# Kernel tuning notes

Hardware: AMD Instinct MI355X
Metric: run time of the kernel (lower is better)

## Reference

```python
import jax, jax.numpy as jnp
import numpy as np
from jax import lax

T_MAX, BATCH, CLASSES, L_MAX = 512, 32, 1296, 64
NINF = -jnp.inf


def _align_one(logsm, label, C, R):
    """Monotonic max-probability forced alignment for one sample.
    logsm: [T, V] log-probs, label: [L] int, C=x_len (valid frames), R=label_len.
    Returns per-frame pseudo target [T] (0-padded past C)."""
    T, V = logsm.shape
    L = label.shape[0]
    rows = jnp.arange(L)
    cols = jnp.arange(T)
    # pb[i, j] = logsm[j, label[i]], restricted to the monotonic band i <= j <= C-R+i
    pb = logsm[:, label].T  # [L, T]
    band = (cols[None, :] >= rows[:, None]) & (cols[None, :] <= C - R + rows[:, None]) & (rows[:, None] < R)
    pb = jnp.where(band, pb, NINF)

    # Forward DP over time columns: dp[i,j] = max(dp[i-1,j-1], dp[i,j-1]) + pb[i,j]
    # (strict > for the diagonal move, exactly as the original numpy code).
    dp0 = jnp.where(rows == 0, pb[:, 0], NINF)

    def step(dp, pb_col):
        shifted = jnp.concatenate([jnp.full((1,), NINF, dp.dtype), dp[:-1]])
        choice = shifted > dp  # True -> came from (i-1, j-1)
        dp_new = jnp.where(choice, shifted, dp) + pb_col
        return dp_new, choice

    _, choices = lax.scan(step, dp0, pb.T[1:])  # [T-1, L] bool
    choices = jnp.concatenate([jnp.zeros((1, L), bool), choices], axis=0)  # [T, L]

    # Backtrack from (R-1, C-1); columns j >= C emit padding 0.
    def bstep(row, jc):
        j, ch = jc
        active = j < C
        tgt = jnp.where(active, label[row], 0)
        row_new = jnp.where(active, row - ch[row].astype(row.dtype), row)
        return row_new, tgt

    row0 = (R - 1).astype(jnp.int32)
    _, targets = lax.scan(bstep, row0, (jnp.arange(T), choices), reverse=True)
    return targets  # [T]


def _make_targets(logsm, label, x_len, label_len):
    # logsm: [T, B, V] -> targets [T, B]
    return jax.vmap(_align_one, in_axes=(1, 0, 0, 0))(logsm, label, x_len, label_len).T


def setup_inputs() -> dict:
    key = jax.random.key(0)
    k0, k1, k2, k3, k4 = jax.random.split(key, 5)
    pred = jax.random.normal(k0, (T_MAX, BATCH, CLASSES), jnp.float32)
    seq_pred = jax.random.normal(k1, (T_MAX, BATCH, CLASSES), jnp.float32)
    label = jax.random.randint(k2, (BATCH, L_MAX), 0, CLASSES)
    x_len = jax.random.randint(k3, (BATCH,), T_MAX // 2, T_MAX + 1)  # >= L_MAX so band is valid
    label_len = jax.random.randint(k4, (BATCH,), 8, L_MAX + 1)
    return {"pred": pred, "seq_pred": seq_pred, "label": label, "x_len": x_len, "label_len": label_len}


def reference(pred, seq_pred, label, x_len, label_len):
    T, B, V = pred.shape
    logsm_seq = jax.nn.log_softmax(seq_pred, axis=-1)
    target = _make_targets(logsm_seq, label, x_len, label_len)  # [T, B] int
    probs = jnp.exp(logsm_seq)  # softmax(seq_pred)
    conf = jnp.take_along_axis(probs, target[..., None], axis=2)[..., 0]  # [T, B]
    smooth = (1.0 - conf) / (V - 1)
    onehot = jax.nn.one_hot(target, V, dtype=pred.dtype)  # [T, B, V]
    true_dist = jnp.where(onehot > 0, conf[..., None], smooth[..., None])
    mask = (jnp.arange(T)[:, None] < x_len[None, :]).astype(pred.dtype)  # [T, B]
    ce = jnp.sum(-true_dist * jax.nn.log_softmax(pred, axis=-1), axis=-1) * mask
    return jnp.mean(ce)
```

## Files before the change

kernel.cpp:

```cpp
#include <hip/hip_runtime.h>

#define T_MAX 512
#define BATCH 32
#define CLASSES 1296
#define L_MAX 64
#define NROWS (T_MAX * BATCH)
#define NV4 (CLASSES / 4)
#define NINF (-INFINITY)

__device__ __forceinline__ float wave_sum64(float v) {
    v += __int_as_float(__builtin_amdgcn_update_dpp(0, __float_as_int(v), 0x111, 0xF, 0xF, true));
    v += __int_as_float(__builtin_amdgcn_update_dpp(0, __float_as_int(v), 0x112, 0xF, 0xF, true));
    v += __int_as_float(__builtin_amdgcn_update_dpp(0, __float_as_int(v), 0x114, 0xF, 0xF, true));
    v += __int_as_float(__builtin_amdgcn_update_dpp(0, __float_as_int(v), 0x118, 0xF, 0xF, true));
    v += __int_as_float(__builtin_amdgcn_update_dpp(0, __float_as_int(v), 0x142, 0xF, 0xF, true));
    v += __int_as_float(__builtin_amdgcn_update_dpp(0, __float_as_int(v), 0x143, 0xF, 0xF, true));
    return v;
}

__global__ __launch_bounds__(256) void rowstats_kernel(
    const float* __restrict__ pred, const float* __restrict__ seqp,
    const int* __restrict__ label,
    float* __restrict__ lse_pred, float* __restrict__ sum_pred,
    float* __restrict__ lse_seq, float* __restrict__ pb, int* __restrict__ counter)
{
    int r = blockIdx.x * 4 + (threadIdx.x >> 6);
    int lane = threadIdx.x & 63;
    if (r == 0 && lane == 0) *counter = 0;
    const float* xp = pred + (size_t)r * CLASSES;
    const float* xs = seqp + (size_t)r * CLASSES;
    const float4* p4 = (const float4*)xp;
    const float4* s4 = (const float4*)xs;

    float4 a0 = p4[lane],       a1 = p4[lane + 64],  a2 = p4[lane + 128];
    float4 a3 = p4[lane + 192], a4 = p4[lane + 256];
    float4 b0 = s4[lane],       b1 = s4[lane + 64],  b2 = s4[lane + 128];
    float4 b3 = s4[lane + 192], b4 = s4[lane + 256];
    float4 at = make_float4(0.f, 0.f, 0.f, 0.f);
    float4 bt = make_float4(0.f, 0.f, 0.f, 0.f);
    if (lane < 4) { at = p4[320 + lane]; bt = s4[320 + lane]; }
    int lab = label[((r & 31) << 6) + lane];

    float sp = __expf(a0.x) + __expf(a0.y) + __expf(a0.z) + __expf(a0.w)
             + __expf(a1.x) + __expf(a1.y) + __expf(a1.z) + __expf(a1.w)
             + __expf(a2.x) + __expf(a2.y) + __expf(a2.z) + __expf(a2.w)
             + __expf(a3.x) + __expf(a3.y) + __expf(a3.z) + __expf(a3.w)
             + __expf(a4.x) + __expf(a4.y) + __expf(a4.z) + __expf(a4.w);
    float sx = (a0.x + a0.y + a0.z + a0.w) + (a1.x + a1.y + a1.z + a1.w)
             + (a2.x + a2.y + a2.z + a2.w) + (a3.x + a3.y + a3.z + a3.w)
             + (a4.x + a4.y + a4.z + a4.w);
    float ss = __expf(b0.x) + __expf(b0.y) + __expf(b0.z) + __expf(b0.w)
             + __expf(b1.x) + __expf(b1.y) + __expf(b1.z) + __expf(b1.w)
             + __expf(b2.x) + __expf(b2.y) + __expf(b2.z) + __expf(b2.w)
             + __expf(b3.x) + __expf(b3.y) + __expf(b3.z) + __expf(b3.w)
             + __expf(b4.x) + __expf(b4.y) + __expf(b4.z) + __expf(b4.w);
    if (lane < 4) {
        sp += __expf(at.x) + __expf(at.y) + __expf(at.z) + __expf(at.w);
        sx += at.x + at.y + at.z + at.w;
        ss += __expf(bt.x) + __expf(bt.y) + __expf(bt.z) + __expf(bt.w);
    }
    sp = wave_sum64(sp);
    sx = wave_sum64(sx);
    ss = wave_sum64(ss);

    int b = r & 31, t = r >> 5;
    pb[(((size_t)(b << 9) + t) << 6) + lane] = xs[lab];
    if (lane == 63) {
        lse_pred[r] = __logf(sp);
        sum_pred[r] = sx;
        lse_seq[r]  = __logf(ss);
    }
}

__global__ __launch_bounds__(128) void align_kernel(
    const float* __restrict__ pb, const int* __restrict__ x_len,
    const int* __restrict__ label_len, int* __restrict__ tg)
{
    int b = blockIdx.x;
    int tid = threadIdx.x, w = tid >> 6, lane = tid & 63;
    int C = x_len[b], R = label_len[b];
    int limit = C - R;
    __shared__ float buf[2][4096];
    __shared__ uint2 chw[8 * 64];
    __shared__ int a_s[64];
    __shared__ int rows_s[T_MAX];
    const float* pbb = pb + ((size_t)b << 15);
    int P = (C + 63) >> 6;

    int l0 = (lane & 15) << 2;
    bool mk0 = (l0 + 0) < R, mk1 = (l0 + 1) < R, mk2 = (l0 + 2) < R, mk3 = (l0 + 3) < R;
    bool isb0 = (lane & 15) == 0;
    const int ninf_i = 0xFF800000;

    if (w == 1) {
        const float4* s4 = (const float4*)pbb;
        float4* d4 = (float4*)buf[0];
        #pragma unroll
        for (int k = 0; k < 16; ++k) {
            float4 q = s4[(k << 6) + lane];
            q.x = mk0 ? q.x : NINF;  q.y = mk1 ? q.y : NINF;
            q.z = mk2 ? q.z : NINF;  q.w = mk3 ? q.w : NINF;
            d4[(k << 6) + lane] = q;
        }
    }
    __syncthreads();

    float dp = NINF;
    for (int p = 0; p < P; ++p) {
        if (w == 1) {
            int ldp = p + 1; if (ldp > 7) ldp = 7;
            const float4* s4 = (const float4*)(pbb + (ldp << 12));
            float4* d4 = (float4*)buf[(p + 1) & 1];
            #pragma unroll
            for (int k = 0; k < 16; ++k) {
                float4 q = s4[(k << 6) + lane];
                q.x = mk0 ? q.x : NINF;  q.y = mk1 ? q.y : NINF;
                q.z = mk2 ? q.z : NINF;  q.w = mk3 ? q.w : NINF;
                d4[(k << 6) + lane] = q;
            }
        } else {
            const float* bc = buf[p & 1];
            int base = p << 6;
            unsigned w0 = 0, w1 = 0;
            #pragma unroll
            for (int g = 0; g < 4; ++g) {
                float v[16];
                #pragma unroll
                for (int u = 0; u < 16; ++u) v[u] = bc[((g << 4) + u) * 64 + lane];
                bool general = (p == 0) || (base + (g << 4) + 15 > limit);
                #pragma unroll
                for (int u = 0; u < 16; ++u) {
                    int kk = (g << 4) + u;
                    int j = base + kk;
                    float val;
                    if (general) {
                        if (p == 0 && kk == 0) {
                            dp = (lane == 0) ? v[0] : NINF;
                            continue;
                        }
                        bool ib = (lane <= j) && (lane >= j - limit);
                        val = ib ? v[u] : NINF;
                    } else {
                        val = v[u];
                    }
                    int dpb = __float_as_int(dp);
                    int t1 = __builtin_amdgcn_update_dpp(ninf_i, dpb, 0x111, 0xF, 0xF, false);
                    int t2 = __builtin_amdgcn_update_dpp(ninf_i, dpb, 0x142, 0xF, 0xF, false);
                    float shifted = __int_as_float(isb0 ? t2 : t1);
                    bool c = shifted > dp;
                    unsigned bit01 = c ? 1u : 0u;
                    if (kk < 32) w0 |= bit01 << kk; else w1 |= bit01 << (kk - 32);
                    dp = fmaxf(shifted, dp) + val;
                }
            }
            chw[(p << 6) + lane] = make_uint2(w0, w1);
        }
        __syncthreads();
    }

    if (tid == 0) {
        const unsigned* ch32 = (const unsigned*)chw;
        int row = R - 1, j = C - 1;
        while (row > 0 && j >= 0) {
            unsigned word = ch32[((j >> 6) << 7) + (row << 1) + ((j >> 5) & 1)];
            unsigned mb = (2u << (j & 31)) - 1;
            unsigned m = word & mb;
            if (m) {
                int hb = 31 - __clz(m);
                int aj = (j & ~31) | hb;
                a_s[row] = aj;
                row--; j = aj - 1;
            } else {
                j = (j & ~31) - 1;
            }
        }
        for (int i = row; i >= 0; --i) a_s[i] = 0;
    }
    __syncthreads();
    if (tid < R) {
        int a = a_s[tid];
        int bi = (tid == R - 1) ? (C - 1) : (a_s[tid + 1] - 1);
        for (int j = a; j <= bi; ++j) rows_s[j] = tid;
    }
    __syncthreads();
    for (int j = tid; j < T_MAX; j += 128)
        tg[(b << 9) + j] = (j < C) ? rows_s[j] : -1;
}

__global__ __launch_bounds__(256) void ce_kernel(
    const float* __restrict__ pred, const int* __restrict__ label,
    const int* __restrict__ x_len,
    const float* __restrict__ lse_pred, const float* __restrict__ sum_pred,
    const float* __restrict__ lse_seq, const float* __restrict__ pb,
    const int* __restrict__ tg, float* __restrict__ partials,
    int* __restrict__ counter, float* __restrict__ out)
{
    int e = blockIdx.x * 256 + threadIdx.x;
    int t = e >> 5, b = e & 31;
    float ce = 0.f;
    if (t < x_len[b]) {
        int row = tg[(b << 9) + t];
        int tgt = label[(b << 6) + row];
        float lp = lse_pred[e];
        float S = sum_pred[e] - (float)CLASSES * lp;
        float lsp_t = pred[(size_t)e * CLASSES + tgt] - lp;
        float conf = __expf(pb[(((size_t)(b << 9) + t) << 6) + row] - lse_seq[e]);
        float smooth = (1.f - conf) * (1.f / (float)(CLASSES - 1));
        ce = -((conf - smooth) * lsp_t + smooth * S);
    }
    ce = wave_sum64(ce);
    __shared__ float sm[4];
    __shared__ int amLast;
    if ((threadIdx.x & 63) == 63) sm[threadIdx.x >> 6] = ce;
    __syncthreads();
    if (threadIdx.x == 0) {
        float p = sm[0] + sm[1] + sm[2] + sm[3];
        __hip_atomic_store(&partials[blockIdx.x], p, __ATOMIC_RELEASE, __HIP_MEMORY_SCOPE_AGENT);
        amLast = (__hip_atomic_fetch_add(counter, 1, __ATOMIC_ACQ_REL, __HIP_MEMORY_SCOPE_AGENT) == 63);
    }
    __syncthreads();
    if (amLast && threadIdx.x < 64) {
        float v = __hip_atomic_load(&partials[threadIdx.x], __ATOMIC_ACQUIRE, __HIP_MEMORY_SCOPE_AGENT);
        for (int o = 32; o; o >>= 1) v += __shfl_down(v, o, 64);
        if (threadIdx.x == 0) out[0] = v * (1.0f / (float)NROWS);
    }
}

extern "C" void kernel_launch(void* const* d_in, const int* in_sizes, int n_in,
                              void* d_out, int out_size, void* d_ws, size_t ws_size,
                              hipStream_t stream) {
    const float* pred      = (const float*)d_in[0];
    const float* seq_pred  = (const float*)d_in[1];
    const int*   label     = (const int*)d_in[2];
    const int*   x_len     = (const int*)d_in[3];
    const int*   label_len = (const int*)d_in[4];
    float* out = (float*)d_out;

    float* w = (float*)d_ws;
    float* lse_pred = w;
    float* sum_pred = w + NROWS;
    float* lse_seq  = w + 2 * NROWS;
    float* pb       = w + 3 * NROWS;
    int*   tg       = (int*)(w + 3 * NROWS + (size_t)BATCH * T_MAX * 64);
    float* partials = (float*)(tg + NROWS);
    int*   counter  = (int*)(partials + 64);

    rowstats_kernel<<<NROWS / 4, 256, 0, stream>>>(pred, seq_pred, label,
                                                   lse_pred, sum_pred, lse_seq, pb, counter);
    align_kernel<<<BATCH, 128, 0, stream>>>(pb, x_len, label_len, tg);
    ce_kernel<<<64, 256, 0, stream>>>(pred, label, x_len,
                                      lse_pred, sum_pred, lse_seq, pb, tg,
                                      partials, counter, out);
}
```

Baseline: 222.5 us.

## Fuse alignment and CE into one single-wave kernel with async LDS loads

Merges the alignment DP kernel and the cross-entropy kernel into one per-sample kernel, which drops a launch and the target round trip through global memory. The block shrinks to a single wave that prefetches the next tile straight into LDS with global_load_lds, synchronised by s_waitcnt instead of __syncthreads, and it no longer loads tiles past the valid length. Label-length masking moves from the copy into the DP itself as an additive bias. The final reduction becomes one float atomic per sample. This leaves only 32 single-wave blocks doing the CE gather, so little parallelism is available there, and the float atomic adds make the summation order nondeterministic.

Result: slower. 230.2 us (+3.5%).

```diff
diff --git a/kernel.cpp b/kernel.cpp
--- a/kernel.cpp
+++ b/kernel.cpp
@@ -18,15 +18,21 @@
     return v;
 }
 
+__device__ __forceinline__ void glds16(const float* g, float* l) {
+    __builtin_amdgcn_global_load_lds((const __attribute__((address_space(1))) void*)g,
+                                     (__attribute__((address_space(3))) void*)l, 16, 0, 0);
+}
+
 __global__ __launch_bounds__(256) void rowstats_kernel(
     const float* __restrict__ pred, const float* __restrict__ seqp,
     const int* __restrict__ label,
     float* __restrict__ lse_pred, float* __restrict__ sum_pred,
-    float* __restrict__ lse_seq, float* __restrict__ pb, int* __restrict__ counter)
+    float* __restrict__ lse_seq, float* __restrict__ pb,
+    int* __restrict__ counter, float* __restrict__ acc)
 {
     int r = blockIdx.x * 4 + (threadIdx.x >> 6);
     int lane = threadIdx.x & 63;
-    if (r == 0 && lane == 0) *counter = 0;
+    if (r == 0 && lane == 0) { *counter = 0; *acc = 0.f; }
     const float* xp = pred + (size_t)r * CLASSES;
     const float* xs = seqp + (size_t)r * CLASSES;
     const float4* p4 = (const float4*)xp;
@@ -72,93 +78,81 @@
     }
 }
 
-__global__ __launch_bounds__(128) void align_kernel(
-    const float* __restrict__ pb, const int* __restrict__ x_len,
-    const int* __restrict__ label_len, int* __restrict__ tg)
+__global__ __launch_bounds__(64) void align_ce_kernel(
+    const float* __restrict__ pb, const float* __restrict__ pred,
+    const int* __restrict__ label, const int* __restrict__ x_len,
+    const int* __restrict__ label_len,
+    const float* __restrict__ lse_pred, const float* __restrict__ sum_pred,
+    const float* __restrict__ lse_seq,
+    float* __restrict__ acc, int* __restrict__ counter, float* __restrict__ out)
 {
-    int b = blockIdx.x;
-    int tid = threadIdx.x, w = tid >> 6, lane = tid & 63;
+    int b = blockIdx.x, lane = threadIdx.x;
     int C = x_len[b], R = label_len[b];
     int limit = C - R;
     __shared__ float buf[2][4096];
-    __shared__ uint2 chw[8 * 64];
+    __shared__ uint2 chw[512];
+    __shared__ int labs[64];
     __shared__ int a_s[64];
     __shared__ int rows_s[T_MAX];
     const float* pbb = pb + ((size_t)b << 15);
     int P = (C + 63) >> 6;
 
-    int l0 = (lane & 15) << 2;
-    bool mk0 = (l0 + 0) < R, mk1 = (l0 + 1) < R, mk2 = (l0 + 2) < R, mk3 = (l0 + 3) < R;
+    labs[lane] = label[(b << 6) + lane];
+    float biasR = (lane < R) ? 0.f : NINF;
     bool isb0 = (lane & 15) == 0;
     const int ninf_i = 0xFF800000;
 
-    if (w == 1) {
-        const float4* s4 = (const float4*)pbb;
-        float4* d4 = (float4*)buf[0];
-        #pragma unroll
-        for (int k = 0; k < 16; ++k) {
-            float4 q = s4[(k << 6) + lane];
-            q.x = mk0 ? q.x : NINF;  q.y = mk1 ? q.y : NINF;
-            q.z = mk2 ? q.z : NINF;  q.w = mk3 ? q.w : NINF;
-            d4[(k << 6) + lane] = q;
-        }
-    }
-    __syncthreads();
+    #pragma unroll
+    for (int k = 0; k < 16; ++k) glds16(pbb + (k << 8) + lane * 4, &buf[0][k << 8]);
 
     float dp = NINF;
     for (int p = 0; p < P; ++p) {
-        if (w == 1) {
-            int ldp = p + 1; if (ldp > 7) ldp = 7;
-            const float4* s4 = (const float4*)(pbb + (ldp << 12));
-            float4* d4 = (float4*)buf[(p + 1) & 1];
+        int ldp = p + 1; if (ldp >= P) ldp = P - 1;
+        const float* src = pbb + ((size_t)ldp << 12);
+        float* dst = buf[(p + 1) & 1];
+        #pragma unroll
+        for (int k = 0; k < 16; ++k) glds16(src + (k << 8) + lane * 4, &dst[k << 8]);
+        __asm__ __volatile__("s_waitcnt vmcnt(16)" ::: "memory");
+
+        const float* bc = buf[p & 1];
+        int base = p << 6;
+        unsigned w0 = 0, w1 = 0;
+        #pragma unroll
+        for (int g = 0; g < 4; ++g) {
+            float v[16];
             #pragma unroll
-            for (int k = 0; k < 16; ++k) {
-                float4 q = s4[(k << 6) + lane];
-                q.x = mk0 ? q.x : NINF;  q.y = mk1 ? q.y : NINF;
-                q.z = mk2 ? q.z : NINF;  q.w = mk3 ? q.w : NINF;
-                d4[(k << 6) + lane] = q;
+            for (int u = 0; u < 16; ++u) v[u] = bc[((g << 4) + u) * 64 + lane];
+            bool general = (p == 0) || (base + (g << 4) + 15 > limit);
+            #pragma unroll
+            for (int u = 0; u < 16; ++u) {
+                int kk = (g << 4) + u;
+                int j = base + kk;
+                float val;
+                if (general) {
+                    if (p == 0 && kk == 0) {
+                        dp = (lane == 0) ? v[0] : NINF;
+                        continue;
+                    }
+                    bool ib = (lane <= j) && (lane >= j - limit) && (lane < R);
+                    val = ib ? v[u] : NINF;
+                } else {
+                    val = v[u] + biasR;
+                }
+                int dpb = __float_as_int(dp);
+                int t1 = __builtin_amdgcn_update_dpp(ninf_i, dpb, 0x111, 0xF, 0xF, false);
+                int t2 = __builtin_amdgcn_update_dpp(ninf_i, dpb, 0x142, 0xF, 0xF, false);
+                float shifted = __int_as_float(isb0 ? t2 : t1);
+                bool c = shifted > dp;
+                unsigned bit01 = c ? 1u : 0u;
+                if (kk < 32) w0 |= bit01 << kk; else w1 |= bit01 << (kk - 32);
+                dp = fmaxf(shifted, dp) + val;
             }
-        } else {
-            const float* bc = buf[p & 1];
-            int base = p << 6;
-            unsigned w0 = 0, w1 = 0;
-            #pragma unroll
-            for (int g = 0; g < 4; ++g) {
-                float v[16];
-                #pragma unroll
-                for (int u = 0; u < 16; ++u) v[u] = bc[((g << 4) + u) * 64 + lane];
-                bool general = (p == 0) || (base + (g << 4) + 15 > limit);
-                #pragma unroll
-                for (int u = 0; u < 16; ++u) {
-                    int kk = (g << 4) + u;
-                    int j = base + kk;
-                    float val;
-                    if (general) {
-                        if (p == 0 && kk == 0) {
-                            dp = (lane == 0) ? v[0] : NINF;
-                            continue;
-                        }
-                        bool ib = (lane <= j) && (lane >= j - limit);
-                        val = ib ? v[u] : NINF;
-                    } else {
-                        val = v[u];
-                    }
-                    int dpb = __float_as_int(dp);
-                    int t1 = __builtin_amdgcn_update_dpp(ninf_i, dpb, 0x111, 0xF, 0xF, false);
-                    int t2 = __builtin_amdgcn_update_dpp(ninf_i, dpb, 0x142, 0xF, 0xF, false);
-                    float shifted = __int_as_float(isb0 ? t2 : t1);
-                    bool c = shifted > dp;
-                    unsigned bit01 = c ? 1u : 0u;
-                    if (kk < 32) w0 |= bit01 << kk; else w1 |= bit01 << (kk - 32);
-                    dp = fmaxf(shifted, dp) + val;
-                }
-            }
-            chw[(p << 6) + lane] = make_uint2(w0, w1);
-        }
-        __syncthreads();
-    }
-
-    if (tid == 0) {
+        }
+        chw[(p << 6) + lane] = make_uint2(w0, w1);
+    }
+    __asm__ __volatile__("s_waitcnt vmcnt(0)" ::: "memory");
+
+    if (lane == 0) {
         const unsigned* ch32 = (const unsigned*)chw;
         int row = R - 1, j = C - 1;
         while (row > 0 && j >= 0) {
@@ -176,53 +170,52 @@
         }
         for (int i = row; i >= 0; --i) a_s[i] = 0;
     }
-    __syncthreads();
-    if (tid < R) {
-        int a = a_s[tid];
-        int bi = (tid == R - 1) ? (C - 1) : (a_s[tid + 1] - 1);
-        for (int j = a; j <= bi; ++j) rows_s[j] = tid;
-    }
-    __syncthreads();
-    for (int j = tid; j < T_MAX; j += 128)
-        tg[(b << 9) + j] = (j < C) ? rows_s[j] : -1;
-}
-
-__global__ __launch_bounds__(256) void ce_kernel(
-    const float* __restrict__ pred, const int* __restrict__ label,
-    const int* __restrict__ x_len,
-    const float* __restrict__ lse_pred, const float* __restrict__ sum_pred,
-    const float* __restrict__ lse_seq, const float* __restrict__ pb,
-    const int* __restrict__ tg, float* __restrict__ partials,
-    int* __restrict__ counter, float* __restrict__ out)
-{
-    int e = blockIdx.x * 256 + threadIdx.x;
-    int t = e >> 5, b = e & 31;
-    float ce = 0.f;
-    if (t < x_len[b]) {
-        int row = tg[(b << 9) + t];
-        int tgt = label[(b << 6) + row];
-        float lp = lse_pred[e];
-        float S = sum_pred[e] - (float)CLASSES * lp;
-        float lsp_t = pred[(size_t)e * CLASSES + tgt] - lp;
-        float conf = __expf(pb[(((size_t)(b << 9) + t) << 6) + row] - lse_seq[e]);
-        float smooth = (1.f - conf) * (1.f / (float)(CLASSES - 1));
-        ce = -((conf - smooth) * lsp_t + smooth * S);
-    }
-    ce = wave_sum64(ce);
-    __shared__ float sm[4];
-    __shared__ int amLast;
-    if ((threadIdx.x & 63) == 63) sm[threadIdx.x >> 6] = ce;
-    __syncthreads();
-    if (threadIdx.x == 0) {
-        float p = sm[0] + sm[1] + sm[2] + sm[3];
-        __hip_atomic_store(&partials[blockIdx.x], p, __ATOMIC_RELEASE, __HIP_MEMORY_SCOPE_AGENT);
-        amLast = (__hip_atomic_fetch_add(counter, 1, __ATOMIC_ACQ_REL, __HIP_MEMORY_SCOPE_AGENT) == 63);
-    }
-    __syncthreads();
-    if (amLast && threadIdx.x < 64) {
-        float v = __hip_atomic_load(&partials[threadIdx.x], __ATOMIC_ACQUIRE, __HIP_MEMORY_SCOPE_AGENT);
-        for (int o = 32; o; o >>= 1) v += __shfl_down(v, o, 64);
-        if (threadIdx.x == 0) out[0] = v * (1.0f / (float)NROWS);
+    if (lane < R) {
+        int a = a_s[lane];
+        int bi = (lane == R - 1) ? (C - 1) : (a_s[lane + 1] - 1);
+        for (int j = a; j <= bi; ++j) rows_s[j] = lane;
+    }
+
+    int row8[8], tgt8[8];
+    float pv[8], pbv[8], lp8[8], sx8[8], lsq8[8];
+    #pragma unroll
+    for (int it = 0; it < 8; ++it) {
+        int t = (it << 6) + lane;
+        row8[it] = (t < C) ? rows_s[t] : 0;
+    }
+    #pragma unroll
+    for (int it = 0; it < 8; ++it) tgt8[it] = labs[row8[it]];
+    #pragma unroll
+    for (int it = 0; it < 8; ++it) {
+        int t = (it << 6) + lane;
+        int e = (t << 5) + b;
+        pv[it]  = pred[(size_t)e * CLASSES + tgt8[it]];
+        pbv[it] = pb[(((size_t)(b << 9) + t) << 6) + row8[it]];
+        lp8[it] = lse_pred[e];
+        sx8[it] = sum_pred[e];
+        lsq8[it] = lse_seq[e];
+    }
+    float ces = 0.f;
+    #pragma unroll
+    for (int it = 0; it < 8; ++it) {
+        int t = (it << 6) + lane;
+        if (t < C) {
+            float lp = lp8[it];
+            float S = sx8[it] - (float)CLASSES * lp;
+            float lsp_t = pv[it] - lp;
+            float conf = __expf(pbv[it] - lsq8[it]);
+            float smooth = (1.f - conf) * (1.f / (float)(CLASSES - 1));
+            ces += -((conf - smooth) * lsp_t + smooth * S);
+        }
+    }
+    ces = wave_sum64(ces);
+    if (lane == 63) {
+        __hip_atomic_fetch_add(acc, ces, __ATOMIC_ACQ_REL, __HIP_MEMORY_SCOPE_AGENT);
+        int c = __hip_atomic_fetch_add(counter, 1, __ATOMIC_ACQ_REL, __HIP_MEMORY_SCOPE_AGENT);
+        if (c == BATCH - 1) {
+            float tot = __hip_atomic_load(acc, __ATOMIC_ACQUIRE, __HIP_MEMORY_SCOPE_AGENT);
+            out[0] = tot * (1.0f / (float)NROWS);
+        }
     }
 }
 
@@ -241,14 +234,13 @@
     float* sum_pred = w + NROWS;
     float* lse_seq  = w + 2 * NROWS;
     float* pb       = w + 3 * NROWS;
-    int*   tg       = (int*)(w + 3 * NROWS + (size_t)BATCH * T_MAX * 64);
-    float* partials = (float*)(tg + NROWS);
-    int*   counter  = (int*)(partials + 64);
+    float* acc      = w + 3 * NROWS + (size_t)BATCH * T_MAX * 64;
+    int*   counter  = (int*)(acc + 1);
 
     rowstats_kernel<<<NROWS / 4, 256, 0, stream>>>(pred, seq_pred, label,
-                                                   lse_pred, sum_pred, lse_seq, pb, counter);
-    align_kernel<<<BATCH, 128, 0, stream>>>(pb, x_len, label_len, tg);
-    ce_kernel<<<64, 256, 0, stream>>>(pred, label, x_len,
-                                      lse_pred, sum_pred, lse_seq, pb, tg,
-                                      partials, counter, out);
-}
+                                                   lse_pred, sum_pred, lse_seq, pb,
+                                                   counter, acc);
+    align_ce_kernel<<<BATCH, 64, 0, stream>>>(pb, pred, label, x_len, label_len,
+                                              lse_pred, sum_pred, lse_seq,
+                                              acc, counter, out);
+}
```

## Overlap serial alignment DP with pred row statistics in one fused launch

Applied to the files above, without the earlier changes.

The pred log-sum-exp and sum work moves out of the first kernel and into a fused kernel. Its first 32 blocks run the per-sample alignment DP while the remaining blocks compute the pred row stats, so the serial DP is hidden behind bandwidth-bound work. The alignment now runs as a single wave that uses global_load_lds async copies with 32-column double buffering instead of a separate loader wave and block barriers. The label-length mask is applied as a bias inside the DP rather than at load time. The cost is scheduling risk: the DP blocks must be dispatched early, and the hand-written vmcnt waits must be correct.

New measurement: 219.4 us. Within noise of the previous version (-1.4%).

```diff
diff --git a/kernel.cpp b/kernel.cpp
--- a/kernel.cpp
+++ b/kernel.cpp
@@ -18,112 +18,81 @@
     return v;
 }
 
-__global__ __launch_bounds__(256) void rowstats_kernel(
-    const float* __restrict__ pred, const float* __restrict__ seqp,
-    const int* __restrict__ label,
-    float* __restrict__ lse_pred, float* __restrict__ sum_pred,
+__device__ __forceinline__ void glds16(const float* g, float* l) {
+    __builtin_amdgcn_global_load_lds((const __attribute__((address_space(1))) void*)g,
+                                     (__attribute__((address_space(3))) void*)l, 16, 0, 0);
+}
+
+__global__ __launch_bounds__(256) void seq_rowstats_kernel(
+    const float* __restrict__ seqp, const int* __restrict__ label,
     float* __restrict__ lse_seq, float* __restrict__ pb, int* __restrict__ counter)
 {
     int r = blockIdx.x * 4 + (threadIdx.x >> 6);
     int lane = threadIdx.x & 63;
     if (r == 0 && lane == 0) *counter = 0;
-    const float* xp = pred + (size_t)r * CLASSES;
     const float* xs = seqp + (size_t)r * CLASSES;
-    const float4* p4 = (const float4*)xp;
     const float4* s4 = (const float4*)xs;
 
-    float4 a0 = p4[lane],       a1 = p4[lane + 64],  a2 = p4[lane + 128];
-    float4 a3 = p4[lane + 192], a4 = p4[lane + 256];
     float4 b0 = s4[lane],       b1 = s4[lane + 64],  b2 = s4[lane + 128];
     float4 b3 = s4[lane + 192], b4 = s4[lane + 256];
-    float4 at = make_float4(0.f, 0.f, 0.f, 0.f);
     float4 bt = make_float4(0.f, 0.f, 0.f, 0.f);
-    if (lane < 4) { at = p4[320 + lane]; bt = s4[320 + lane]; }
+    if (lane < 4) bt = s4[320 + lane];
     int lab = label[((r & 31) << 6) + lane];
 
-    float sp = __expf(a0.x) + __expf(a0.y) + __expf(a0.z) + __expf(a0.w)
-             + __expf(a1.x) + __expf(a1.y) + __expf(a1.z) + __expf(a1.w)
-             + __expf(a2.x) + __expf(a2.y) + __expf(a2.z) + __expf(a2.w)
-             + __expf(a3.x) + __expf(a3.y) + __expf(a3.z) + __expf(a3.w)
-             + __expf(a4.x) + __expf(a4.y) + __expf(a4.z) + __expf(a4.w);
-    float sx = (a0.x + a0.y + a0.z + a0.w) + (a1.x + a1.y + a1.z + a1.w)
-             + (a2.x + a2.y + a2.z + a2.w) + (a3.x + a3.y + a3.z + a3.w)
-             + (a4.x + a4.y + a4.z + a4.w);
     float ss = __expf(b0.x) + __expf(b0.y) + __expf(b0.z) + __expf(b0.w)
              + __expf(b1.x) + __expf(b1.y) + __expf(b1.z) + __expf(b1.w)
              + __expf(b2.x) + __expf(b2.y) + __expf(b2.z) + __expf(b2.w)
              + __expf(b3.x) + __expf(b3.y) + __expf(b3.z) + __expf(b3.w)
              + __expf(b4.x) + __expf(b4.y) + __expf(b4.z) + __expf(b4.w);
-    if (lane < 4) {
-        sp += __expf(at.x) + __expf(at.y) + __expf(at.z) + __expf(at.w);
-        sx += at.x + at.y + at.z + at.w;
+    if (lane < 4)
         ss += __expf(bt.x) + __expf(bt.y) + __expf(bt.z) + __expf(bt.w);
-    }
-    sp = wave_sum64(sp);
-    sx = wave_sum64(sx);
     ss = wave_sum64(ss);
 
     int b = r & 31, t = r >> 5;
     pb[(((size_t)(b << 9) + t) << 6) + lane] = xs[lab];
-    if (lane == 63) {
-        lse_pred[r] = __logf(sp);
-        sum_pred[r] = sx;
-        lse_seq[r]  = __logf(ss);
-    }
-}
-
-__global__ __launch_bounds__(128) void align_kernel(
-    const float* __restrict__ pb, const int* __restrict__ x_len,
-    const int* __restrict__ label_len, int* __restrict__ tg)
+    if (lane == 63) lse_seq[r] = __logf(ss);
+}
+
+__global__ __launch_bounds__(256) void fused_align_pred_kernel(
+    const float* __restrict__ pred, const float* __restrict__ pb,
+    const int* __restrict__ x_len, const int* __restrict__ label_len,
+    float* __restrict__ lse_pred, float* __restrict__ sum_pred,
+    int* __restrict__ tg)
 {
-    int b = blockIdx.x;
-    int tid = threadIdx.x, w = tid >> 6, lane = tid & 63;
-    int C = x_len[b], R = label_len[b];
-    int limit = C - R;
-    __shared__ float buf[2][4096];
-    __shared__ uint2 chw[8 * 64];
+    __shared__ float abuf[2][2048];
+    __shared__ unsigned chw[1024];
     __shared__ int a_s[64];
     __shared__ int rows_s[T_MAX];
-    const float* pbb = pb + ((size_t)b << 15);
-    int P = (C + 63) >> 6;
-
-    int l0 = (lane & 15) << 2;
-    bool mk0 = (l0 + 0) < R, mk1 = (l0 + 1) < R, mk2 = (l0 + 2) < R, mk3 = (l0 + 3) < R;
-    bool isb0 = (lane & 15) == 0;
-    const int ninf_i = 0xFF800000;
-
-    if (w == 1) {
-        const float4* s4 = (const float4*)pbb;
-        float4* d4 = (float4*)buf[0];
+
+    if (blockIdx.x < 32) {
+        if (threadIdx.x >= 64) return;
+        int b = blockIdx.x, lane = threadIdx.x;
+        int C = x_len[b], R = label_len[b];
+        int limit = C - R;
+        const float* pbb = pb + ((size_t)b << 15);
+        int P = (C + 31) >> 5;
+
+        float biasR = (lane < R) ? 0.f : NINF;
+        bool isb0 = (lane & 15) == 0;
+        const int ninf_i = 0xFF800000;
+
         #pragma unroll
-        for (int k = 0; k < 16; ++k) {
-            float4 q = s4[(k << 6) + lane];
-            q.x = mk0 ? q.x : NINF;  q.y = mk1 ? q.y : NINF;
-            q.z = mk2 ? q.z : NINF;  q.w = mk3 ? q.w : NINF;
-            d4[(k << 6) + lane] = q;
-        }
-    }
-    __syncthreads();
-
-    float dp = NINF;
-    for (int p = 0; p < P; ++p) {
-        if (w == 1) {
-            int ldp = p + 1; if (ldp > 7) ldp = 7;
-            const float4* s4 = (const float4*)(pbb + (ldp << 12));
-            float4* d4 = (float4*)buf[(p + 1) & 1];
+        for (int k = 0; k < 8; ++k) glds16(pbb + (k << 8) + lane * 4, &abuf[0][k << 8]);
+
+        float dp = NINF;
+        for (int p = 0; p < P; ++p) {
+            int ldp = p + 1; if (ldp >= P) ldp = P - 1;
+            const float* src = pbb + ((size_t)ldp << 11);
+            float* dst = abuf[(p + 1) & 1];
             #pragma unroll
-            for (int k = 0; k < 16; ++k) {
-                float4 q = s4[(k << 6) + lane];
-                q.x = mk0 ? q.x : NINF;  q.y = mk1 ? q.y : NINF;
-                q.z = mk2 ? q.z : NINF;  q.w = mk3 ? q.w : NINF;
-                d4[(k << 6) + lane] = q;
-            }
-        } else {
-            const float* bc = buf[p & 1];
-            int base = p << 6;
-            unsigned w0 = 0, w1 = 0;
+            for (int k = 0; k < 8; ++k) glds16(src + (k << 8) + lane * 4, &dst[k << 8]);
+            __asm__ __volatile__("s_waitcnt vmcnt(8)" ::: "memory");
+
+            const float* bc = abuf[p & 1];
+            int base = p << 5;
+            unsigned w0 = 0;
             #pragma unroll
-            for (int g = 0; g < 4; ++g) {
+            for (int g = 0; g < 2; ++g) {
                 float v[16];
                 #pragma unroll
                 for (int u = 0; u < 16; ++u) v[u] = bc[((g << 4) + u) * 64 + lane];
@@ -138,53 +107,78 @@
                             dp = (lane == 0) ? v[0] : NINF;
                             continue;
                         }
-                        bool ib = (lane <= j) && (lane >= j - limit);
+                        bool ib = (lane <= j) && (lane >= j - limit) && (lane < R);
                         val = ib ? v[u] : NINF;
                     } else {
-                        val = v[u];
+                        val = v[u] + biasR;
                     }
                     int dpb = __float_as_int(dp);
                     int t1 = __builtin_amdgcn_update_dpp(ninf_i, dpb, 0x111, 0xF, 0xF, false);
                     int t2 = __builtin_amdgcn_update_dpp(ninf_i, dpb, 0x142, 0xF, 0xF, false);
                     float shifted = __int_as_float(isb0 ? t2 : t1);
                     bool c = shifted > dp;
-                    unsigned bit01 = c ? 1u : 0u;
-                    if (kk < 32) w0 |= bit01 << kk; else w1 |= bit01 << (kk - 32);
+                    w0 |= (c ? 1u : 0u) << kk;
                     dp = fmaxf(shifted, dp) + val;
                 }
             }
-            chw[(p << 6) + lane] = make_uint2(w0, w1);
-        }
-        __syncthreads();
-    }
-
-    if (tid == 0) {
-        const unsigned* ch32 = (const unsigned*)chw;
-        int row = R - 1, j = C - 1;
-        while (row > 0 && j >= 0) {
-            unsigned word = ch32[((j >> 6) << 7) + (row << 1) + ((j >> 5) & 1)];
-            unsigned mb = (2u << (j & 31)) - 1;
-            unsigned m = word & mb;
-            if (m) {
-                int hb = 31 - __clz(m);
-                int aj = (j & ~31) | hb;
-                a_s[row] = aj;
-                row--; j = aj - 1;
-            } else {
-                j = (j & ~31) - 1;
+            chw[(p << 6) + lane] = w0;
+        }
+        __asm__ __volatile__("s_waitcnt vmcnt(0)" ::: "memory");
+
+        if (lane == 0) {
+            int row = R - 1, j = C - 1;
+            while (row > 0 && j >= 0) {
+                unsigned word = chw[((j >> 5) << 6) + row];
+                unsigned mb = (2u << (j & 31)) - 1;
+                unsigned m = word & mb;
+                if (m) {
+                    int hb = 31 - __clz(m);
+                    int aj = (j & ~31) | hb;
+                    a_s[row] = aj;
+                    row--; j = aj - 1;
+                } else {
+                    j = (j & ~31) - 1;
+                }
             }
-        }
-        for (int i = row; i >= 0; --i) a_s[i] = 0;
-    }
-    __syncthreads();
-    if (tid < R) {
-        int a = a_s[tid];
-        int bi = (tid == R - 1) ? (C - 1) : (a_s[tid + 1] - 1);
-        for (int j = a; j <= bi; ++j) rows_s[j] = tid;
-    }
-    __syncthreads();
-    for (int j = tid; j < T_MAX; j += 128)
-        tg[(b << 9) + j] = (j < C) ? rows_s[j] : -1;
+            for (int i = row; i >= 0; --i) a_s[i] = 0;
+        }
+        if (lane < R) {
+            int a = a_s[lane];
+            int bi = (lane == R - 1) ? (C - 1) : (a_s[lane + 1] - 1);
+            for (int j = a; j <= bi; ++j) rows_s[j] = lane;
+        }
+        for (int j = lane; j < T_MAX; j += 64)
+            tg[(b << 9) + j] = (j < C) ? rows_s[j] : -1;
+    } else {
+        int r = (blockIdx.x - 32) * 4 + (threadIdx.x >> 6);
+        int lane = threadIdx.x & 63;
+        const float* xp = pred + (size_t)r * CLASSES;
+        const float4* p4 = (const float4*)xp;
+
+        float4 a0 = p4[lane],       a1 = p4[lane + 64],  a2 = p4[lane + 128];
+        float4 a3 = p4[lane + 192], a4 = p4[lane + 256];
+        float4 at = make_float4(0.f, 0.f, 0.f, 0.f);
+        if (lane < 4) at = p4[320 + lane];
+
+        float sp = __expf(a0.x) + __expf(a0.y) + __expf(a0.z) + __expf(a0.w)
+                 + __expf(a1.x) + __expf(a1.y) + __expf(a1.z) + __expf(a1.w)
+                 + __expf(a2.x) + __expf(a2.y) + __expf(a2.z) + __expf(a2.w)
+                 + __expf(a3.x) + __expf(a3.y) + __expf(a3.z) + __expf(a3.w)
+                 + __expf(a4.x) + __expf(a4.y) + __expf(a4.z) + __expf(a4.w);
+        float sx = (a0.x + a0.y + a0.z + a0.w) + (a1.x + a1.y + a1.z + a1.w)
+                 + (a2.x + a2.y + a2.z + a2.w) + (a3.x + a3.y + a3.z + a3.w)
+                 + (a4.x + a4.y + a4.z + a4.w);
+        if (lane < 4) {
+            sp += __expf(at.x) + __expf(at.y) + __expf(at.z) + __expf(at.w);
+            sx += at.x + at.y + at.z + at.w;
+        }
+        sp = wave_sum64(sp);
+        sx = wave_sum64(sx);
+        if (lane == 63) {
+            lse_pred[r] = __logf(sp);
+            sum_pred[r] = sx;
+        }
+    }
 }
 
 __global__ __launch_bounds__(256) void ce_kernel(
@@ -245,9 +239,11 @@
     float* partials = (float*)(tg + NROWS);
     int*   counter  = (int*)(partials + 64);
 
-    rowstats_kernel<<<NROWS / 4, 256, 0, stream>>>(pred, seq_pred, label,
-                                                   lse_pred, sum_pred, lse_seq, pb, counter);
-    align_kernel<<<BATCH, 128, 0, stream>>>(pb, x_len, label_len, tg);
+    seq_rowstats_kernel<<<NROWS / 4, 256, 0, stream>>>(seq_pred, label,
+                                                       lse_seq, pb, counter);
+    fused_align_pred_kernel<<<32 + NROWS / 4, 256, 0, stream>>>(pred, pb,
+                                                                x_len, label_len,
+                                                                lse_pred, sum_pred, tg);
     ce_kernel<<<64, 256, 0, stream>>>(pred, label, x_len,
                                       lse_pred, sum_pred, lse_seq, pb, tg,
                                       partials, counter, out);
```
